# Kernel optimization log

Hardware: AMD Instinct MI355X
Metric: run time of the kernel (lower is better)

The kernel has to match this reference:

```python
import jax, jax.numpy as jnp
import numpy as np

TOKENS_B, TOKENS_S, N_IN, N_OUT = 8, 2048, 4096, 4096
N8, N4 = 2048, 2048  # channels per format


def setup_inputs() -> dict:
    key = jax.random.key(0)
    k = jax.random.split(key, 7)
    x = jax.random.normal(k[0], (TOKENS_B, TOKENS_S, N_IN), dtype=jnp.float32)
    # int8-format group: values in [-128, 127], per-output-channel scale
    q8 = jax.random.randint(k[1], (N8, N_IN), -128, 128, dtype=jnp.int32)
    s8 = jax.random.uniform(k[2], (N8, 1), dtype=jnp.float32) * 0.01 + 1e-4
    # int4-format group: values in [-8, 7], per-output-channel scale
    q4 = jax.random.randint(k[3], (N4, N_IN), -8, 8, dtype=jnp.int32)
    s4 = jax.random.uniform(k[4], (N4, 1), dtype=jnp.float32) * 0.1 + 1e-4
    # inverse permutation restoring original channel order from [fmt8 | fmt4] concat
    inv_perm = jax.random.permutation(k[5], N_OUT).astype(jnp.int32)
    bias = jax.random.normal(k[6], (N_OUT,), dtype=jnp.float32) * 0.01
    return {"x": x, "q8": q8, "s8": s8, "q4": q4, "s4": s4,
            "inv_perm": inv_perm, "bias": bias}


def reference(x, q8, s8, q4, s4, inv_perm, bias):
    # Per-format dequantize: w = q * scale (per-output-channel scale)
    w8 = q8.astype(jnp.float32) * s8  # [N8, N_IN]
    w4 = q4.astype(jnp.float32) * s4  # [N4, N_IN]
    # Grouped GEMMs, one per format
    y8 = jnp.einsum('bsi,oi->bso', x, w8)  # [B, S, N8]
    y4 = jnp.einsum('bsi,oi->bso', x, w4)  # [B, S, N4]
    # Concat along output channels, then restore original channel order
    y = jnp.concatenate([y8, y4], axis=-1)  # [B, S, N_OUT]
    out = y[..., inv_perm] + bias
    return out
```

## Files before the change

kernel.cpp:

```cpp
#include <hip/hip_runtime.h>


#define M_TOK 16384
#define N_O   4096
#define K_IN  4096
#define N8F   2048
#define NT    (K_IN / 128)

typedef __attribute__((ext_vector_type(4))) int i32x4;

__device__ __forceinline__ void gl_lds16(const void* g, void* l) {
  __builtin_amdgcn_global_load_lds(
      (const __attribute__((address_space(1))) unsigned int*)g,
      (__attribute__((address_space(3))) unsigned int*)l, 16, 0, 0);
}

__device__ __forceinline__ int clampq(float f) {
  int q = (int)rintf(f);
  return q > 127 ? 127 : (q < -127 ? -127 : q);
}

__global__ void prep_kernel(const float* __restrict__ x,
                            const int4* __restrict__ q8, const float* __restrict__ s8,
                            const int4* __restrict__ q4, const float* __restrict__ s4,
                            const int* __restrict__ inv,
                            char* __restrict__ Wq, float* __restrict__ scale,
                            float* __restrict__ sx, char* __restrict__ xq) {
  __shared__ float red[4];
  const int t = threadIdx.x;
  if (blockIdx.x < N_O) {
    const int j = blockIdx.x;
    const int c = inv[j];
    const int4* src; float s;
    if (c < N8F) { src = q8 + (size_t)c * (K_IN / 4);         s = s8[c]; }
    else         { src = q4 + (size_t)(c - N8F) * (K_IN / 4); s = s4[c - N8F]; }
    if (t == 0) scale[j] = s;
    unsigned dw[4];
#pragma unroll
    for (int i = 0; i < 4; ++i) {
      int4 v = src[t * 4 + i];
      dw[i] = (v.x & 255) | ((v.y & 255) << 8) | ((v.z & 255) << 16)
            | ((unsigned)(v.w & 255) << 24);
    }
    *(uint4*)(Wq + (size_t)j * K_IN + t * 16) = make_uint4(dw[0], dw[1], dw[2], dw[3]);
  } else {
    const int T = blockIdx.x - N_O;
    const float4* xr = (const float4*)(x + (size_t)T * K_IN);
    float4 v[4];
    float m = 0.f;
#pragma unroll
    for (int i = 0; i < 4; ++i) {
      v[i] = xr[t * 4 + i];
      m = fmaxf(m, fmaxf(fmaxf(fabsf(v[i].x), fabsf(v[i].y)),
                         fmaxf(fabsf(v[i].z), fabsf(v[i].w))));
    }
#pragma unroll
    for (int o = 32; o; o >>= 1) m = fmaxf(m, __shfl_xor(m, o));
    if ((t & 63) == 0) red[t >> 6] = m;
    __syncthreads();
    m = fmaxf(fmaxf(red[0], red[1]), fmaxf(red[2], red[3]));
    const float rq = m > 0.f ? 127.f / m : 0.f;
    if (t == 0) sx[T] = m * (1.f / 127.f);
    unsigned dw[4];
#pragma unroll
    for (int i = 0; i < 4; ++i) {
      int a0 = clampq(v[i].x * rq), a1 = clampq(v[i].y * rq);
      int a2 = clampq(v[i].z * rq), a3 = clampq(v[i].w * rq);
      dw[i] = (a0 & 255) | ((a1 & 255) << 8) | ((a2 & 255) << 16)
            | ((unsigned)(a3 & 255) << 24);
    }
    *(uint4*)(xq + (size_t)T * K_IN + t * 16) = make_uint4(dw[0], dw[1], dw[2], dw[3]);
  }
}

__global__ __launch_bounds__(512, 2)
void gemm_i8(const char* __restrict__ xq, const char* __restrict__ Wq,
             const float* __restrict__ sx, const float* __restrict__ scale,
             const float* __restrict__ bias, float* __restrict__ out) {
  __shared__ __align__(16) char sm[131072];
  const int t = threadIdx.x;
  const int w = t >> 6, l = t & 63;
  const int wr = w >> 2, wc = w & 3;
  const int bm = blockIdx.x >> 4, bn = blockIdx.x & 15;
  const int row0 = bm * 256, col0 = bn * 256;

  const int srow = l >> 3;
  const int schunk = ((l & 7) ^ srow) * 16;
  const char* aG = xq + (size_t)(row0 + w * 16 + srow) * K_IN + schunk;
  const char* bG = Wq + (size_t)(col0 + w * 16 + srow) * K_IN + schunk;
  char* aL0 = sm + w * 2048;
  char* bL0 = sm + 32768 + w * 2048;

  auto stage = [&](int buf, int kt) {
    const int o = kt << 7;
    char* aD = aL0 + buf * 65536;
    char* bD = bL0 + buf * 65536;
    gl_lds16(aG + o, aD);
    gl_lds16(aG + 32768 + o, aD + 1024);
    gl_lds16(aG + 524288 + o, aD + 16384);
    gl_lds16(aG + 524288 + 32768 + o, aD + 17408);
    gl_lds16(bG + o, bD);
    gl_lds16(bG + 32768 + o, bD + 1024);
    gl_lds16(bG + 524288 + o, bD + 16384);
    gl_lds16(bG + 524288 + 32768 + o, bD + 17408);
  };

  const int lrow128 = (l & 15) * 128;
  const int cb0 = (((l >> 4) << 4) ^ ((l & 7) << 4));
  const char* rA0  = sm + wr * 16384 + lrow128 + cb0;
  const char* rA0x = sm + wr * 16384 + lrow128 + (cb0 ^ 64);
  const char* rB0  = sm + 32768 + (wc >> 1) * 16384 + (wc & 1) * 8192 + lrow128 + cb0;
  const char* rB0x = sm + 32768 + (wc >> 1) * 16384 + (wc & 1) * 8192 + lrow128 + (cb0 ^ 64);

  i32x4 acc[8][4];
#pragma unroll
  for (int m = 0; m < 8; ++m)
#pragma unroll
    for (int n = 0; n < 4; ++n) acc[m][n] = (i32x4){0, 0, 0, 0};

  stage(0, 0);
  __syncthreads();

  for (int kt2 = 0; kt2 < NT; kt2 += 2) {
#pragma unroll
    for (int half = 0; half < 2; ++half) {
      const int kt = kt2 + half;
      const int cur = half;
      const char* rA  = rA0 + cur * 65536;
      const char* rAx = rA0x + cur * 65536;
      const char* rB  = rB0 + cur * 65536;
      const char* rBx = rB0x + cur * 65536;

      if (kt + 1 < NT) stage(cur ^ 1, kt + 1);

      i32x4 b0[4], b1[4], a0[4], a1[4];
#pragma unroll
      for (int n = 0; n < 4; ++n) {
        b0[n] = *(const i32x4*)(rB + n * 2048);
        b1[n] = *(const i32x4*)(rBx + n * 2048);
      }
#pragma unroll
      for (int m = 0; m < 4; ++m) a0[m] = *(const i32x4*)(rA + m * 2048);
#pragma unroll
      for (int m = 0; m < 4; ++m)
#pragma unroll
        for (int n = 0; n < 4; ++n)
          acc[m][n] = __builtin_amdgcn_mfma_i32_16x16x64_i8(a0[m], b0[n],
                                                            acc[m][n], 0, 0, 0);
#pragma unroll
      for (int m = 0; m < 4; ++m) a1[m] = *(const i32x4*)(rAx + m * 2048);
#pragma unroll
      for (int m = 0; m < 4; ++m)
#pragma unroll
        for (int n = 0; n < 4; ++n)
          acc[m][n] = __builtin_amdgcn_mfma_i32_16x16x64_i8(a1[m], b1[n],
                                                            acc[m][n], 0, 0, 0);
#pragma unroll
      for (int m = 0; m < 4; ++m) a0[m] = *(const i32x4*)(rA + (4 + m) * 2048);
#pragma unroll
      for (int m = 0; m < 4; ++m)
#pragma unroll
        for (int n = 0; n < 4; ++n)
          acc[4 + m][n] = __builtin_amdgcn_mfma_i32_16x16x64_i8(a0[m], b0[n],
                                                                acc[4 + m][n], 0, 0, 0);
#pragma unroll
      for (int m = 0; m < 4; ++m) a1[m] = *(const i32x4*)(rAx + (4 + m) * 2048);
#pragma unroll
      for (int m = 0; m < 4; ++m)
#pragma unroll
        for (int n = 0; n < 4; ++n)
          acc[4 + m][n] = __builtin_amdgcn_mfma_i32_16x16x64_i8(a1[m], b1[n],
                                                                acc[4 + m][n], 0, 0, 0);

      __syncthreads();
    }
  }

  const int orow0 = row0 + wr * 128 + ((l >> 4) << 2);
  const int ocol0 = col0 + wc * 64 + (l & 15);
#pragma unroll
  for (int n = 0; n < 4; ++n) {
    const int col = ocol0 + n * 16;
    const float sc = scale[col];
    const float bi = bias[col];
#pragma unroll
    for (int m = 0; m < 8; ++m) {
      const int r = orow0 + m * 16;
      const float4 sxv = *(const float4*)(sx + r);
      out[(size_t)(r + 0) * N_O + col] = (float)acc[m][n][0] * (sxv.x * sc) + bi;
      out[(size_t)(r + 1) * N_O + col] = (float)acc[m][n][1] * (sxv.y * sc) + bi;
      out[(size_t)(r + 2) * N_O + col] = (float)acc[m][n][2] * (sxv.z * sc) + bi;
      out[(size_t)(r + 3) * N_O + col] = (float)acc[m][n][3] * (sxv.w * sc) + bi;
    }
  }
}

extern "C" void kernel_launch(void* const* d_in, const int* in_sizes, int n_in,
                              void* d_out, int out_size, void* d_ws, size_t ws_size,
                              hipStream_t stream) {
  const float* x    = (const float*)d_in[0];
  const int*   q8   = (const int*)d_in[1];
  const float* s8   = (const float*)d_in[2];
  const int*   q4   = (const int*)d_in[3];
  const float* s4   = (const float*)d_in[4];
  const int*   inv  = (const int*)d_in[5];
  const float* bias = (const float*)d_in[6];
  float* out = (float*)d_out;

  char* ws = (char*)d_ws;
  char*  Wq    = ws;
  float* scale = (float*)(ws + (size_t)N_O * K_IN);
  float* sx    = (float*)(ws + (size_t)N_O * K_IN + 65536);
  char*  xq    = ws + (size_t)N_O * K_IN + 65536 + 65536;

  prep_kernel<<<N_O + M_TOK, 256, 0, stream>>>(x, (const int4*)q8, s8,
                                               (const int4*)q4, s4, inv,
                                               Wq, scale, sx, xq);
  gemm_i8<<<(M_TOK / 256) * (N_O / 256), 512, 0, stream>>>(xq, Wq, sx, scale,
                                                           bias, out);
}
```

Before: 383.8 us.

## Use 4 waves per block with 128x128 per-wave tiles in int8 GEMM

Halves the GEMM block to 256 threads (2x2 waves) so each wave computes a 128x128 output sub-tile with 64 accumulator fragments instead of 32. Each wave now loads twice as many staging chunks, and every A and B fragment read from LDS feeds more MFMAs, lowering LDS traffic per MFMA. The cost is much higher register pressure (256 accumulator VGPRs), and launch bounds drop to one block per SM, so fewer waves are left to hide latency.

Measured after the change: 528.0 us. +37.5%, slower.

```diff
diff --git a/kernel.cpp b/kernel.cpp
--- a/kernel.cpp
+++ b/kernel.cpp
@@ -73,50 +73,49 @@
   }
 }
 
-__global__ __launch_bounds__(512, 2)
+__global__ __launch_bounds__(256, 1)
 void gemm_i8(const char* __restrict__ xq, const char* __restrict__ Wq,
              const float* __restrict__ sx, const float* __restrict__ scale,
              const float* __restrict__ bias, float* __restrict__ out) {
   __shared__ __align__(16) char sm[131072];
   const int t = threadIdx.x;
   const int w = t >> 6, l = t & 63;
-  const int wr = w >> 2, wc = w & 3;
+  const int wr = w >> 1, wc = w & 1;
   const int bm = blockIdx.x >> 4, bn = blockIdx.x & 15;
   const int row0 = bm * 256, col0 = bn * 256;
 
   const int srow = l >> 3;
   const int schunk = ((l & 7) ^ srow) * 16;
-  const char* aG = xq + (size_t)(row0 + w * 16 + srow) * K_IN + schunk;
-  const char* bG = Wq + (size_t)(col0 + w * 16 + srow) * K_IN + schunk;
-  char* aL0 = sm + w * 2048;
-  char* bL0 = sm + 32768 + w * 2048;
+  const char* aG = xq + (size_t)(row0 + w * 32 + srow) * K_IN + schunk;
+  const char* bG = Wq + (size_t)(col0 + w * 32 + srow) * K_IN + schunk;
+  char* aL0 = sm + w * 4096;
+  char* bL0 = sm + 32768 + w * 4096;
 
   auto stage = [&](int buf, int kt) {
     const int o = kt << 7;
     char* aD = aL0 + buf * 65536;
     char* bD = bL0 + buf * 65536;
-    gl_lds16(aG + o, aD);
-    gl_lds16(aG + 32768 + o, aD + 1024);
-    gl_lds16(aG + 524288 + o, aD + 16384);
-    gl_lds16(aG + 524288 + 32768 + o, aD + 17408);
-    gl_lds16(bG + o, bD);
-    gl_lds16(bG + 32768 + o, bD + 1024);
-    gl_lds16(bG + 524288 + o, bD + 16384);
-    gl_lds16(bG + 524288 + 32768 + o, bD + 17408);
+#pragma unroll
+    for (int i = 0; i < 4; ++i) {
+      gl_lds16(aG + (size_t)(8 * i) * K_IN + o, aD + i * 1024);
+      gl_lds16(aG + (size_t)(128 + 8 * i) * K_IN + o, aD + 16384 + i * 1024);
+      gl_lds16(bG + (size_t)(8 * i) * K_IN + o, bD + i * 1024);
+      gl_lds16(bG + (size_t)(128 + 8 * i) * K_IN + o, bD + 16384 + i * 1024);
+    }
   };
 
   const int lrow128 = (l & 15) * 128;
   const int cb0 = (((l >> 4) << 4) ^ ((l & 7) << 4));
   const char* rA0  = sm + wr * 16384 + lrow128 + cb0;
   const char* rA0x = sm + wr * 16384 + lrow128 + (cb0 ^ 64);
-  const char* rB0  = sm + 32768 + (wc >> 1) * 16384 + (wc & 1) * 8192 + lrow128 + cb0;
-  const char* rB0x = sm + 32768 + (wc >> 1) * 16384 + (wc & 1) * 8192 + lrow128 + (cb0 ^ 64);
-
-  i32x4 acc[8][4];
+  const char* rB0  = sm + 32768 + wc * 16384 + lrow128 + cb0;
+  const char* rB0x = sm + 32768 + wc * 16384 + lrow128 + (cb0 ^ 64);
+
+  i32x4 acc[8][8];
 #pragma unroll
   for (int m = 0; m < 8; ++m)
 #pragma unroll
-    for (int n = 0; n < 4; ++n) acc[m][n] = (i32x4){0, 0, 0, 0};
+    for (int n = 0; n < 8; ++n) acc[m][n] = (i32x4){0, 0, 0, 0};
 
   stage(0, 0);
   __syncthreads();
@@ -126,60 +125,56 @@
     for (int half = 0; half < 2; ++half) {
       const int kt = kt2 + half;
       const int cur = half;
-      const char* rA  = rA0 + cur * 65536;
-      const char* rAx = rA0x + cur * 65536;
-      const char* rB  = rB0 + cur * 65536;
-      const char* rBx = rB0x + cur * 65536;
-
       if (kt + 1 < NT) stage(cur ^ 1, kt + 1);
 
-      i32x4 b0[4], b1[4], a0[4], a1[4];
-#pragma unroll
-      for (int n = 0; n < 4; ++n) {
-        b0[n] = *(const i32x4*)(rB + n * 2048);
-        b1[n] = *(const i32x4*)(rBx + n * 2048);
+      {
+        const char* rA = rA0 + cur * 65536;
+        const char* rB = rB0 + cur * 65536;
+        i32x4 b[8];
+#pragma unroll
+        for (int n = 0; n < 8; ++n) b[n] = *(const i32x4*)(rB + n * 2048);
+#pragma unroll
+        for (int mp = 0; mp < 4; ++mp) {
+          i32x4 a0 = *(const i32x4*)(rA + (2 * mp) * 2048);
+          i32x4 a1 = *(const i32x4*)(rA + (2 * mp + 1) * 2048);
+#pragma unroll
+          for (int n = 0; n < 8; ++n)
+            acc[2 * mp][n] = __builtin_amdgcn_mfma_i32_16x16x64_i8(a0, b[n],
+                                                acc[2 * mp][n], 0, 0, 0);
+#pragma unroll
+          for (int n = 0; n < 8; ++n)
+            acc[2 * mp + 1][n] = __builtin_amdgcn_mfma_i32_16x16x64_i8(a1, b[n],
+                                                acc[2 * mp + 1][n], 0, 0, 0);
+        }
       }
-#pragma unroll
-      for (int m = 0; m < 4; ++m) a0[m] = *(const i32x4*)(rA + m * 2048);
-#pragma unroll
-      for (int m = 0; m < 4; ++m)
-#pragma unroll
-        for (int n = 0; n < 4; ++n)
-          acc[m][n] = __builtin_amdgcn_mfma_i32_16x16x64_i8(a0[m], b0[n],
-                                                            acc[m][n], 0, 0, 0);
-#pragma unroll
-      for (int m = 0; m < 4; ++m) a1[m] = *(const i32x4*)(rAx + m * 2048);
-#pragma unroll
-      for (int m = 0; m < 4; ++m)
-#pragma unroll
-        for (int n = 0; n < 4; ++n)
-          acc[m][n] = __builtin_amdgcn_mfma_i32_16x16x64_i8(a1[m], b1[n],
-                                                            acc[m][n], 0, 0, 0);
-#pragma unroll
-      for (int m = 0; m < 4; ++m) a0[m] = *(const i32x4*)(rA + (4 + m) * 2048);
-#pragma unroll
-      for (int m = 0; m < 4; ++m)
-#pragma unroll
-        for (int n = 0; n < 4; ++n)
-          acc[4 + m][n] = __builtin_amdgcn_mfma_i32_16x16x64_i8(a0[m], b0[n],
-                                                                acc[4 + m][n], 0, 0, 0);
-#pragma unroll
-      for (int m = 0; m < 4; ++m) a1[m] = *(const i32x4*)(rAx + (4 + m) * 2048);
-#pragma unroll
-      for (int m = 0; m < 4; ++m)
-#pragma unroll
-        for (int n = 0; n < 4; ++n)
-          acc[4 + m][n] = __builtin_amdgcn_mfma_i32_16x16x64_i8(a1[m], b1[n],
-                                                                acc[4 + m][n], 0, 0, 0);
-
+      {
+        const char* rA = rA0x + cur * 65536;
+        const char* rB = rB0x + cur * 65536;
+        i32x4 b[8];
+#pragma unroll
+        for (int n = 0; n < 8; ++n) b[n] = *(const i32x4*)(rB + n * 2048);
+#pragma unroll
+        for (int mp = 0; mp < 4; ++mp) {
+          i32x4 a0 = *(const i32x4*)(rA + (2 * mp) * 2048);
+          i32x4 a1 = *(const i32x4*)(rA + (2 * mp + 1) * 2048);
+#pragma unroll
+          for (int n = 0; n < 8; ++n)
+            acc[2 * mp][n] = __builtin_amdgcn_mfma_i32_16x16x64_i8(a0, b[n],
+                                                acc[2 * mp][n], 0, 0, 0);
+#pragma unroll
+          for (int n = 0; n < 8; ++n)
+            acc[2 * mp + 1][n] = __builtin_amdgcn_mfma_i32_16x16x64_i8(a1, b[n],
+                                                acc[2 * mp + 1][n], 0, 0, 0);
+        }
+      }
       __syncthreads();
     }
   }
 
   const int orow0 = row0 + wr * 128 + ((l >> 4) << 2);
-  const int ocol0 = col0 + wc * 64 + (l & 15);
-#pragma unroll
-  for (int n = 0; n < 4; ++n) {
+  const int ocol0 = col0 + wc * 128 + (l & 15);
+#pragma unroll
+  for (int n = 0; n < 8; ++n) {
     const int col = ocol0 + n * 16;
     const float sc = scale[col];
     const float bi = bias[col];
@@ -216,6 +211,6 @@
   prep_kernel<<<N_O + M_TOK, 256, 0, stream>>>(x, (const int4*)q8, s8,
                                                (const int4*)q4, s4, inv,
                                                Wq, scale, sx, xq);
-  gemm_i8<<<(M_TOK / 256) * (N_O / 256), 512, 0, stream>>>(xq, Wq, sx, scale,
+  gemm_i8<<<(M_TOK / 256) * (N_O / 256), 256, 0, stream>>>(xq, Wq, sx, scale,
                                                            bias, out);
 }
```
